# Kernel tuning notes

Hardware: AMD Instinct MI355X
Metric: run time of the kernel (lower is better)

The kernel has to match this reference:

```python
import jax, jax.numpy as jnp
import numpy as np

N_NODES = 50000
EPS = 1e-16
NEG_SLOPE = 0.2


def _gat_conv(x, src, dst, W, a_src, a_dst, bias, heads, out_c, concat, n):
    # Linear transform: [N, heads, out_c]
    h = (x @ W).reshape(n, heads, out_c)
    # Per-node attention logits (split form of PyG's 'a' vector)
    al_src = jnp.einsum('nhc,hc->nh', h, a_src)  # [N, H]
    al_dst = jnp.einsum('nhc,hc->nh', h, a_dst)  # [N, H]
    # Edge-wise scores, softmax over incoming edges of each destination
    e = jax.nn.leaky_relu(al_src[src] + al_dst[dst], NEG_SLOPE)  # [E, H]
    m = jax.ops.segment_max(e, dst, num_segments=n)              # [N, H]
    ex = jnp.exp(e - m[dst])
    s = jax.ops.segment_sum(ex, dst, num_segments=n)             # [N, H]
    alpha = ex / (s[dst] + EPS)                                  # [E, H]
    # Attention-weighted scatter-aggregate of source features
    out = jax.ops.segment_sum(h[src] * alpha[:, :, None], dst, num_segments=n)
    if concat:
        out = out.reshape(n, heads * out_c)
    else:
        out = out.mean(axis=1)
    return out + bias


def _add_self_loops(edge_index, n):
    loop = jnp.arange(n, dtype=edge_index.dtype)
    src = jnp.concatenate([edge_index[0], loop])
    dst = jnp.concatenate([edge_index[1], loop])
    return src, dst


def setup_inputs() -> dict:
    key = jax.random.key(0)
    ks = jax.random.split(key, 10)
    n, e = N_NODES, 640000
    x = jax.random.normal(ks[0], (n, 128), dtype=jnp.float32)
    edge_index = jax.random.randint(ks[1], (2, e), 0, n, dtype=jnp.int64)
    sc = 0.1
    return {
        'x': x,
        'edge_index': edge_index,
        'W1': jax.random.normal(ks[2], (128, 256), dtype=jnp.float32) * sc,
        'a1_src': jax.random.normal(ks[3], (8, 32), dtype=jnp.float32) * sc,
        'a1_dst': jax.random.normal(ks[4], (8, 32), dtype=jnp.float32) * sc,
        'b1': jax.random.normal(ks[5], (256,), dtype=jnp.float32) * sc,
        'W2': jax.random.normal(ks[6], (256, 64), dtype=jnp.float32) * sc,
        'a2_src': jax.random.normal(ks[7], (1, 64), dtype=jnp.float32) * sc,
        'a2_dst': jax.random.normal(ks[8], (1, 64), dtype=jnp.float32) * sc,
        'b2': jax.random.normal(ks[9], (64,), dtype=jnp.float32) * sc,
    }


def reference(x, edge_index, W1, a1_src, a1_dst, b1, W2, a2_src, a2_dst, b2):
    n = x.shape[0]
    src, dst = _add_self_loops(edge_index, n)  # PyG GATConv add_self_loops=True
    # Dropouts are identity in eval mode.
    h = _gat_conv(x, src, dst, W1, a1_src, a1_dst, b1, heads=8, out_c=32, concat=True, n=n)
    h = jax.nn.elu(h)
    out = _gat_conv(h, src, dst, W2, a2_src, a2_dst, b2, heads=1, out_c=64, concat=False, n=n)
    return out
```

## Files before the change

### kernel.cpp

```cpp
#include <hip/hip_runtime.h>


static __device__ __forceinline__ float lrelu(float x) { return x > 0.f ? x : 0.2f * x; }

__global__ void count_deg(const int* __restrict__ dstv, int* __restrict__ deg, int E) {
  int e = blockIdx.x * blockDim.x + threadIdx.x;
  if (e < E) atomicAdd(&deg[dstv[e]], 1);
}

__global__ void scan_partial(const int* __restrict__ deg, int* __restrict__ off,
                             int* __restrict__ bsum, int n) {
  int tid = threadIdx.x;
  int i = blockIdx.x * 256 + tid;
  int v = (i < n) ? deg[i] : 0;
  int lane = tid & 63, w = tid >> 6;
  int sv = v;
#pragma unroll
  for (int o = 1; o < 64; o <<= 1) {
    int t = __shfl_up(sv, o);
    if (lane >= o) sv += t;
  }
  __shared__ int ws[4];
  if (lane == 63) ws[w] = sv;
  __syncthreads();
  int add = 0;
  for (int j = 0; j < w; ++j) add += ws[j];
  sv += add;
  if (i < n) off[i + 1] = sv;
  if (tid == 255) bsum[blockIdx.x] = sv;
}

__global__ void scan_bsum(int* __restrict__ bsum, int* __restrict__ off, int nb) {
  int tid = threadIdx.x;
  int v = (tid < nb) ? bsum[tid] : 0;
  int lane = tid & 63, w = tid >> 6;
  int sv = v;
#pragma unroll
  for (int o = 1; o < 64; o <<= 1) {
    int t = __shfl_up(sv, o);
    if (lane >= o) sv += t;
  }
  __shared__ int ws[4];
  if (lane == 63) ws[w] = sv;
  __syncthreads();
  int add = 0;
  for (int j = 0; j < w; ++j) add += ws[j];
  sv += add;
  if (tid < nb) bsum[tid] = sv - v;
  if (tid == 0) off[0] = 0;
}

__global__ void add_carry(const int* __restrict__ deg, int* __restrict__ off,
                          const int* __restrict__ bsum, int* __restrict__ cur, int n) {
  int i = blockIdx.x * 256 + threadIdx.x;
  if (i < n) {
    int o = off[i + 1] + bsum[blockIdx.x];
    off[i + 1] = o;
    cur[i] = o - deg[i];
  }
}

__global__ void fill_csr(const int* __restrict__ srcv, const int* __restrict__ dstv,
                         int* __restrict__ cur, int* __restrict__ csr,
                         int* __restrict__ csr_dst, int E) {
  int e = blockIdx.x * blockDim.x + threadIdx.x;
  if (e < E) {
    int d = dstv[e];
    int p = atomicAdd(&cur[d], 1);
    csr[p] = srcv[e];
    csr_dst[p] = d;
  }
}

__global__ __launch_bounds__(256) void gemm1(const float* __restrict__ x, const float* __restrict__ W,
                                             float* __restrict__ h, int n) {
  __shared__ float xs[32][64];
  __shared__ float Ws[32][256];
  int tid = threadIdx.x;
  int tc = tid & 31;
  int tr = tid >> 5;
  int lr = tid & 63, lj = tid >> 6;
  int r0 = blockIdx.x * 64;

  float acc[8][8];
#pragma unroll
  for (int r = 0; r < 8; ++r)
#pragma unroll
    for (int j = 0; j < 8; ++j) acc[r][j] = 0.f;

  for (int k0 = 0; k0 < 128; k0 += 32) {
    __syncthreads();
    {
      int rr = r0 + lr;
      float4 v0 = {0, 0, 0, 0}, v1 = {0, 0, 0, 0};
      if (rr < n) {
        const float* p = x + (size_t)rr * 128 + k0 + lj * 8;
        v0 = *(const float4*)p;
        v1 = *(const float4*)(p + 4);
      }
      int kk = lj * 8;
      xs[kk + 0][lr] = v0.x; xs[kk + 1][lr] = v0.y; xs[kk + 2][lr] = v0.z; xs[kk + 3][lr] = v0.w;
      xs[kk + 4][lr] = v1.x; xs[kk + 5][lr] = v1.y; xs[kk + 6][lr] = v1.z; xs[kk + 7][lr] = v1.w;
    }
    {
      const float4* src = (const float4*)(W + (size_t)k0 * 256);
      float4* dst = (float4*)&Ws[0][0];
#pragma unroll
      for (int i = tid; i < 2048; i += 256) dst[i] = src[i];
    }
    __syncthreads();
#pragma unroll 4
    for (int k = 0; k < 32; ++k) {
      float xv[8];
      *(float4*)&xv[0] = *(const float4*)&xs[k][tr * 8];
      *(float4*)&xv[4] = *(const float4*)&xs[k][tr * 8 + 4];
      float wv[8];
#pragma unroll
      for (int j = 0; j < 8; ++j) wv[j] = Ws[k][tc + 32 * j];
#pragma unroll
      for (int r = 0; r < 8; ++r)
#pragma unroll
        for (int j = 0; j < 8; ++j) acc[r][j] = fmaf(xv[r], wv[j], acc[r][j]);
    }
  }
#pragma unroll
  for (int r = 0; r < 8; ++r) {
    int row = r0 + tr * 8 + r;
    if (row < n) {
#pragma unroll
      for (int j = 0; j < 8; ++j) h[(size_t)row * 256 + tc + 32 * j] = acc[r][j];
    }
  }
}

__global__ __launch_bounds__(256) void gemm2(const float* __restrict__ xin, const float* __restrict__ W,
                                             float* __restrict__ h, int n) {
  __shared__ float xs[32][128];
  __shared__ float Ws[32][64];
  int tid = threadIdx.x;
  int tc = tid & 15;
  int tr = tid >> 4;
  int r0 = blockIdx.x * 128;

  float acc[8][4];
#pragma unroll
  for (int r = 0; r < 8; ++r)
#pragma unroll
    for (int j = 0; j < 4; ++j) acc[r][j] = 0.f;

  for (int k0 = 0; k0 < 256; k0 += 32) {
    __syncthreads();
#pragma unroll
    for (int idx = tid; idx < 1024; idx += 256) {
      int r = idx & 127, q = idx >> 7;
      int rr = r0 + r;
      float4 v = {0, 0, 0, 0};
      if (rr < n) v = *(const float4*)(xin + (size_t)rr * 256 + k0 + q * 4);
      int kk = q * 4;
      xs[kk + 0][r] = v.x; xs[kk + 1][r] = v.y; xs[kk + 2][r] = v.z; xs[kk + 3][r] = v.w;
    }
    {
      const float4* src = (const float4*)(W + (size_t)k0 * 64);
      float4* dst = (float4*)&Ws[0][0];
#pragma unroll
      for (int i = tid; i < 512; i += 256) dst[i] = src[i];
    }
    __syncthreads();
#pragma unroll 4
    for (int k = 0; k < 32; ++k) {
      float xv[8];
      *(float4*)&xv[0] = *(const float4*)&xs[k][tr * 8];
      *(float4*)&xv[4] = *(const float4*)&xs[k][tr * 8 + 4];
      float wv[4];
#pragma unroll
      for (int j = 0; j < 4; ++j) wv[j] = Ws[k][tc + 16 * j];
#pragma unroll
      for (int r = 0; r < 8; ++r)
#pragma unroll
        for (int j = 0; j < 4; ++j) acc[r][j] = fmaf(xv[r], wv[j], acc[r][j]);
    }
  }
#pragma unroll
  for (int r = 0; r < 8; ++r) {
    int row = r0 + tr * 8 + r;
    if (row < n) {
#pragma unroll
      for (int j = 0; j < 4; ++j) h[(size_t)row * 64 + tc + 16 * j] = acc[r][j];
    }
  }
}

__global__ __launch_bounds__(256) void logits1(const float* __restrict__ h, const float* __restrict__ as,
                                               const float* __restrict__ ad, float* __restrict__ als,
                                               float* __restrict__ ald, int n) {
  int node = blockIdx.x * 4 + (threadIdx.x >> 6);
  int lane = threadIdx.x & 63;
  if (node >= n) return;
  float4 v = *(const float4*)&h[(size_t)node * 256 + lane * 4];
  float4 cs = *(const float4*)&as[lane * 4];
  float4 cd = *(const float4*)&ad[lane * 4];
  float ps = v.x * cs.x + v.y * cs.y + v.z * cs.z + v.w * cs.w;
  float pd = v.x * cd.x + v.y * cd.y + v.z * cd.z + v.w * cd.w;
#pragma unroll
  for (int o = 1; o < 8; o <<= 1) {
    ps += __shfl_xor(ps, o);
    pd += __shfl_xor(pd, o);
  }
  if ((lane & 7) == 0) {
    int head = lane >> 3;
    als[node * 8 + head] = ps;
    ald[node * 8 + head] = pd;
  }
}

__global__ __launch_bounds__(256) void logits2(const float* __restrict__ h, const float* __restrict__ as,
                                               const float* __restrict__ ad, float* __restrict__ als,
                                               float* __restrict__ ald, int n) {
  int node = blockIdx.x * 4 + (threadIdx.x >> 6);
  int lane = threadIdx.x & 63;
  if (node >= n) return;
  float v = h[(size_t)node * 64 + lane];
  float ps = v * as[lane];
  float pd = v * ad[lane];
#pragma unroll
  for (int o = 1; o < 64; o <<= 1) {
    ps += __shfl_xor(ps, o);
    pd += __shfl_xor(pd, o);
  }
  if (lane == 0) {
    als[node] = ps;
    ald[node] = pd;
  }
}

__global__ __launch_bounds__(256) void alpha1_k(const float* __restrict__ als, const float* __restrict__ ald,
                                                const int* __restrict__ csr, const int* __restrict__ csr_dst,
                                                float* __restrict__ alpha, int E) {
  int idx = blockIdx.x * 256 + threadIdx.x;
  if (idx >= E * 8) return;
  int p = idx >> 3, hd = idx & 7;
  int s = csr[p], d = csr_dst[p];
  alpha[idx] = expf(lrelu(als[s * 8 + hd] + ald[d * 8 + hd]));
}

__global__ __launch_bounds__(256) void alpha2_k(const float* __restrict__ als, const float* __restrict__ ald,
                                                const int* __restrict__ csr, const int* __restrict__ csr_dst,
                                                float* __restrict__ alpha, int E) {
  int p = blockIdx.x * 256 + threadIdx.x;
  if (p >= E) return;
  alpha[p] = expf(lrelu(als[csr[p]] + ald[csr_dst[p]]));
}

__global__ __launch_bounds__(256) void agg1(const float* __restrict__ h, const float* __restrict__ alpha,
                                            const float* __restrict__ als, const float* __restrict__ ald,
                                            const int* __restrict__ off, const int* __restrict__ csr,
                                            const float* __restrict__ bias, float* __restrict__ outp, int n) {
  int d = blockIdx.x * 4 + (threadIdx.x >> 6);
  if (d >= n) return;
  int lane = threadIdx.x & 63;
  int head = lane >> 3;
  float w0 = expf(lrelu(als[d * 8 + head] + ald[d * 8 + head]));
  float4 hv = *(const float4*)&h[(size_t)d * 256 + lane * 4];
  float4 acc;
  acc.x = w0 * hv.x; acc.y = w0 * hv.y; acc.z = w0 * hv.z; acc.w = w0 * hv.w;
  float wsum = w0;
  int beg = off[d], end = off[d + 1];
  int i = beg;
  for (; i + 1 < end; i += 2) {
    int s0 = csr[i], s1 = csr[i + 1];
    float wa = alpha[(size_t)i * 8 + head];
    float wb = alpha[(size_t)(i + 1) * 8 + head];
    float4 h0 = *(const float4*)&h[(size_t)s0 * 256 + lane * 4];
    float4 h1 = *(const float4*)&h[(size_t)s1 * 256 + lane * 4];
    acc.x = fmaf(wa, h0.x, acc.x); acc.y = fmaf(wa, h0.y, acc.y);
    acc.z = fmaf(wa, h0.z, acc.z); acc.w = fmaf(wa, h0.w, acc.w);
    acc.x = fmaf(wb, h1.x, acc.x); acc.y = fmaf(wb, h1.y, acc.y);
    acc.z = fmaf(wb, h1.z, acc.z); acc.w = fmaf(wb, h1.w, acc.w);
    wsum += wa + wb;
  }
  if (i < end) {
    int s = csr[i];
    float w = alpha[(size_t)i * 8 + head];
    float4 h0 = *(const float4*)&h[(size_t)s * 256 + lane * 4];
    acc.x = fmaf(w, h0.x, acc.x); acc.y = fmaf(w, h0.y, acc.y);
    acc.z = fmaf(w, h0.z, acc.z); acc.w = fmaf(w, h0.w, acc.w);
    wsum += w;
  }
  float inv = 1.f / (wsum + 1e-16f);
  float4 b = *(const float4*)&bias[lane * 4];
  float4 o;
  o.x = acc.x * inv + b.x; o.y = acc.y * inv + b.y;
  o.z = acc.z * inv + b.z; o.w = acc.w * inv + b.w;
  o.x = o.x > 0.f ? o.x : expm1f(o.x);
  o.y = o.y > 0.f ? o.y : expm1f(o.y);
  o.z = o.z > 0.f ? o.z : expm1f(o.z);
  o.w = o.w > 0.f ? o.w : expm1f(o.w);
  *(float4*)&outp[(size_t)d * 256 + lane * 4] = o;
}

__global__ __launch_bounds__(256) void agg2(const float* __restrict__ h, const float* __restrict__ alpha,
                                            const float* __restrict__ als, const float* __restrict__ ald,
                                            const int* __restrict__ off, const int* __restrict__ csr,
                                            const float* __restrict__ bias, float* __restrict__ outp, int n) {
  int d = blockIdx.x * 4 + (threadIdx.x >> 6);
  if (d >= n) return;
  int c = threadIdx.x & 63;
  float w0 = expf(lrelu(als[d] + ald[d]));
  float acc = w0 * h[(size_t)d * 64 + c];
  float wsum = w0;
  int beg = off[d], end = off[d + 1];
  int i = beg;
  for (; i + 1 < end; i += 2) {
    int s0 = csr[i], s1 = csr[i + 1];
    float wa = alpha[i];
    float wb = alpha[i + 1];
    float h0 = h[(size_t)s0 * 64 + c];
    float h1 = h[(size_t)s1 * 64 + c];
    acc = fmaf(wa, h0, acc);
    acc = fmaf(wb, h1, acc);
    wsum += wa + wb;
  }
  if (i < end) {
    int s = csr[i];
    float w = alpha[i];
    acc = fmaf(w, h[(size_t)s * 64 + c], acc);
    wsum += w;
  }
  outp[(size_t)d * 64 + c] = acc / (wsum + 1e-16f) + bias[c];
}

extern "C" void kernel_launch(void* const* d_in, const int* in_sizes, int n_in,
                              void* d_out, int out_size, void* d_ws, size_t ws_size,
                              hipStream_t stream) {
  const float* x  = (const float*)d_in[0];
  const int* ei   = (const int*)d_in[1];
  const float* W1 = (const float*)d_in[2];
  const float* a1s = (const float*)d_in[3];
  const float* a1d = (const float*)d_in[4];
  const float* b1  = (const float*)d_in[5];
  const float* W2  = (const float*)d_in[6];
  const float* a2s = (const float*)d_in[7];
  const float* a2d = (const float*)d_in[8];
  const float* b2  = (const float*)d_in[9];
  float* outp = (float*)d_out;

  int n = in_sizes[0] / 128;
  int E = in_sizes[1] / 2;
  const int* srcv = ei;
  const int* dstv = ei + E;

  char* wsb = (char*)d_ws;
  size_t p = 0;
  auto alloc = [&](size_t bytes) -> char* {
    char* r = wsb + p;
    p += (bytes + 511) & ~size_t(511);
    return r;
  };
  int* deg  = (int*)alloc((size_t)n * 4);
  int* off  = (int*)alloc(((size_t)n + 1) * 4);
  int* cur  = (int*)alloc((size_t)n * 4);
  int* bsum = (int*)alloc(1024);
  int* csr  = (int*)alloc((size_t)E * 4);
  int* csrd = (int*)alloc((size_t)E * 4);
  float* h1   = (float*)alloc((size_t)n * 256 * 4);
  float* al1s = (float*)alloc((size_t)n * 8 * 4);
  float* al1d = (float*)alloc((size_t)n * 8 * 4);
  float* o1   = (float*)alloc((size_t)n * 256 * 4);
  float* h2   = (float*)alloc((size_t)n * 64 * 4);
  float* al2s = (float*)alloc((size_t)n * 4);
  float* al2d = (float*)alloc((size_t)n * 4);
  float* alp1 = (float*)alloc((size_t)E * 8 * 4);
  float* alp2 = (float*)alloc((size_t)E * 4);
  (void)ws_size;

  hipMemsetAsync(deg, 0, (size_t)n * 4, stream);
  int eb = (E + 255) / 256;
  int nb = (n + 255) / 256;
  count_deg<<<eb, 256, 0, stream>>>(dstv, deg, E);
  scan_partial<<<nb, 256, 0, stream>>>(deg, off, bsum, n);
  scan_bsum<<<1, 256, 0, stream>>>(bsum, off, nb);
  add_carry<<<nb, 256, 0, stream>>>(deg, off, bsum, cur, n);
  fill_csr<<<eb, 256, 0, stream>>>(srcv, dstv, cur, csr, csrd, E);

  gemm1<<<(n + 63) / 64, 256, 0, stream>>>(x, W1, h1, n);
  logits1<<<(n + 3) / 4, 256, 0, stream>>>(h1, a1s, a1d, al1s, al1d, n);
  alpha1_k<<<(E * 8 + 255) / 256, 256, 0, stream>>>(al1s, al1d, csr, csrd, alp1, E);
  agg1<<<(n + 3) / 4, 256, 0, stream>>>(h1, alp1, al1s, al1d, off, csr, b1, o1, n);
  gemm2<<<(n + 127) / 128, 256, 0, stream>>>(o1, W2, h2, n);
  logits2<<<(n + 3) / 4, 256, 0, stream>>>(h2, a2s, a2d, al2s, al2d, n);
  alpha2_k<<<eb, 256, 0, stream>>>(al2s, al2d, csr, csrd, alp2, E);
  agg2<<<(n + 3) / 4, 256, 0, stream>>>(h2, alp2, al2s, al2d, off, csr, b2, outp, n);
}
```

Measured before the change: 436.8 us.

## Fuse edge attention weight computation into aggregation kernels, drop alpha buffers

Removes the separate alpha1/alpha2 kernels and the per-edge alpha and csr_dst arrays, and computes exp(leaky_relu(als[src]+ald[dst])) inline inside the aggregation loops. This avoids writing and re-reading E*8 and E floats plus the destination-index array, and drops two launches. In exchange each lane recomputes the exp redundantly and does an extra gather of als per source. The aggregation loops are also unrolled from 2 to 4 edges to expose more memory-level parallelism.

```diff
diff --git a/kernel.cpp b/kernel.cpp
--- a/kernel.cpp
+++ b/kernel.cpp
@@ -61,14 +61,11 @@
 }
 
 __global__ void fill_csr(const int* __restrict__ srcv, const int* __restrict__ dstv,
-                         int* __restrict__ cur, int* __restrict__ csr,
-                         int* __restrict__ csr_dst, int E) {
+                         int* __restrict__ cur, int* __restrict__ csr, int E) {
   int e = blockIdx.x * blockDim.x + threadIdx.x;
   if (e < E) {
-    int d = dstv[e];
-    int p = atomicAdd(&cur[d], 1);
+    int p = atomicAdd(&cur[dstv[e]], 1);
     csr[p] = srcv[e];
-    csr_dst[p] = d;
   }
 }
 
@@ -233,25 +230,7 @@
   }
 }
 
-__global__ __launch_bounds__(256) void alpha1_k(const float* __restrict__ als, const float* __restrict__ ald,
-                                                const int* __restrict__ csr, const int* __restrict__ csr_dst,
-                                                float* __restrict__ alpha, int E) {
-  int idx = blockIdx.x * 256 + threadIdx.x;
-  if (idx >= E * 8) return;
-  int p = idx >> 3, hd = idx & 7;
-  int s = csr[p], d = csr_dst[p];
-  alpha[idx] = expf(lrelu(als[s * 8 + hd] + ald[d * 8 + hd]));
-}
-
-__global__ __launch_bounds__(256) void alpha2_k(const float* __restrict__ als, const float* __restrict__ ald,
-                                                const int* __restrict__ csr, const int* __restrict__ csr_dst,
-                                                float* __restrict__ alpha, int E) {
-  int p = blockIdx.x * 256 + threadIdx.x;
-  if (p >= E) return;
-  alpha[p] = expf(lrelu(als[csr[p]] + ald[csr_dst[p]]));
-}
-
-__global__ __launch_bounds__(256) void agg1(const float* __restrict__ h, const float* __restrict__ alpha,
+__global__ __launch_bounds__(256) void agg1(const float* __restrict__ h,
                                             const float* __restrict__ als, const float* __restrict__ ald,
                                             const int* __restrict__ off, const int* __restrict__ csr,
                                             const float* __restrict__ bias, float* __restrict__ outp, int n) {
@@ -259,28 +238,41 @@
   if (d >= n) return;
   int lane = threadIdx.x & 63;
   int head = lane >> 3;
-  float w0 = expf(lrelu(als[d * 8 + head] + ald[d * 8 + head]));
+  float ad = ald[d * 8 + head];
+  float w0 = expf(lrelu(als[d * 8 + head] + ad));
   float4 hv = *(const float4*)&h[(size_t)d * 256 + lane * 4];
   float4 acc;
   acc.x = w0 * hv.x; acc.y = w0 * hv.y; acc.z = w0 * hv.z; acc.w = w0 * hv.w;
   float wsum = w0;
   int beg = off[d], end = off[d + 1];
   int i = beg;
-  for (; i + 1 < end; i += 2) {
-    int s0 = csr[i], s1 = csr[i + 1];
-    float wa = alpha[(size_t)i * 8 + head];
-    float wb = alpha[(size_t)(i + 1) * 8 + head];
+  for (; i + 3 < end; i += 4) {
+    int s0 = csr[i], s1 = csr[i + 1], s2 = csr[i + 2], s3 = csr[i + 3];
+    float a0 = als[s0 * 8 + head];
+    float a1 = als[s1 * 8 + head];
+    float a2 = als[s2 * 8 + head];
+    float a3 = als[s3 * 8 + head];
     float4 h0 = *(const float4*)&h[(size_t)s0 * 256 + lane * 4];
     float4 h1 = *(const float4*)&h[(size_t)s1 * 256 + lane * 4];
+    float4 h2 = *(const float4*)&h[(size_t)s2 * 256 + lane * 4];
+    float4 h3 = *(const float4*)&h[(size_t)s3 * 256 + lane * 4];
+    float wa = expf(lrelu(a0 + ad));
+    float wb = expf(lrelu(a1 + ad));
+    float wc = expf(lrelu(a2 + ad));
+    float wd = expf(lrelu(a3 + ad));
     acc.x = fmaf(wa, h0.x, acc.x); acc.y = fmaf(wa, h0.y, acc.y);
     acc.z = fmaf(wa, h0.z, acc.z); acc.w = fmaf(wa, h0.w, acc.w);
     acc.x = fmaf(wb, h1.x, acc.x); acc.y = fmaf(wb, h1.y, acc.y);
     acc.z = fmaf(wb, h1.z, acc.z); acc.w = fmaf(wb, h1.w, acc.w);
-    wsum += wa + wb;
-  }
-  if (i < end) {
+    acc.x = fmaf(wc, h2.x, acc.x); acc.y = fmaf(wc, h2.y, acc.y);
+    acc.z = fmaf(wc, h2.z, acc.z); acc.w = fmaf(wc, h2.w, acc.w);
+    acc.x = fmaf(wd, h3.x, acc.x); acc.y = fmaf(wd, h3.y, acc.y);
+    acc.z = fmaf(wd, h3.z, acc.z); acc.w = fmaf(wd, h3.w, acc.w);
+    wsum += (wa + wb) + (wc + wd);
+  }
+  for (; i < end; ++i) {
     int s = csr[i];
-    float w = alpha[(size_t)i * 8 + head];
+    float w = expf(lrelu(als[s * 8 + head] + ad));
     float4 h0 = *(const float4*)&h[(size_t)s * 256 + lane * 4];
     acc.x = fmaf(w, h0.x, acc.x); acc.y = fmaf(w, h0.y, acc.y);
     acc.z = fmaf(w, h0.z, acc.z); acc.w = fmaf(w, h0.w, acc.w);
@@ -298,31 +290,42 @@
   *(float4*)&outp[(size_t)d * 256 + lane * 4] = o;
 }
 
-__global__ __launch_bounds__(256) void agg2(const float* __restrict__ h, const float* __restrict__ alpha,
+__global__ __launch_bounds__(256) void agg2(const float* __restrict__ h,
                                             const float* __restrict__ als, const float* __restrict__ ald,
                                             const int* __restrict__ off, const int* __restrict__ csr,
                                             const float* __restrict__ bias, float* __restrict__ outp, int n) {
   int d = blockIdx.x * 4 + (threadIdx.x >> 6);
   if (d >= n) return;
   int c = threadIdx.x & 63;
-  float w0 = expf(lrelu(als[d] + ald[d]));
+  float ad = ald[d];
+  float w0 = expf(lrelu(als[d] + ad));
   float acc = w0 * h[(size_t)d * 64 + c];
   float wsum = w0;
   int beg = off[d], end = off[d + 1];
   int i = beg;
-  for (; i + 1 < end; i += 2) {
-    int s0 = csr[i], s1 = csr[i + 1];
-    float wa = alpha[i];
-    float wb = alpha[i + 1];
+  for (; i + 3 < end; i += 4) {
+    int s0 = csr[i], s1 = csr[i + 1], s2 = csr[i + 2], s3 = csr[i + 3];
+    float a0 = als[s0];
+    float a1 = als[s1];
+    float a2 = als[s2];
+    float a3 = als[s3];
     float h0 = h[(size_t)s0 * 64 + c];
     float h1 = h[(size_t)s1 * 64 + c];
+    float h2 = h[(size_t)s2 * 64 + c];
+    float h3 = h[(size_t)s3 * 64 + c];
+    float wa = expf(lrelu(a0 + ad));
+    float wb = expf(lrelu(a1 + ad));
+    float wc = expf(lrelu(a2 + ad));
+    float wd = expf(lrelu(a3 + ad));
     acc = fmaf(wa, h0, acc);
     acc = fmaf(wb, h1, acc);
-    wsum += wa + wb;
-  }
-  if (i < end) {
+    acc = fmaf(wc, h2, acc);
+    acc = fmaf(wd, h3, acc);
+    wsum += (wa + wb) + (wc + wd);
+  }
+  for (; i < end; ++i) {
     int s = csr[i];
-    float w = alpha[i];
+    float w = expf(lrelu(als[s] + ad));
     acc = fmaf(w, h[(size_t)s * 64 + c], acc);
     wsum += w;
   }
@@ -361,7 +364,6 @@
   int* cur  = (int*)alloc((size_t)n * 4);
   int* bsum = (int*)alloc(1024);
   int* csr  = (int*)alloc((size_t)E * 4);
-  int* csrd = (int*)alloc((size_t)E * 4);
   float* h1   = (float*)alloc((size_t)n * 256 * 4);
   float* al1s = (float*)alloc((size_t)n * 8 * 4);
   float* al1d = (float*)alloc((size_t)n * 8 * 4);
@@ -369,8 +371,6 @@
   float* h2   = (float*)alloc((size_t)n * 64 * 4);
   float* al2s = (float*)alloc((size_t)n * 4);
   float* al2d = (float*)alloc((size_t)n * 4);
-  float* alp1 = (float*)alloc((size_t)E * 8 * 4);
-  float* alp2 = (float*)alloc((size_t)E * 4);
   (void)ws_size;
 
   hipMemsetAsync(deg, 0, (size_t)n * 4, stream);
@@ -380,14 +380,12 @@
   scan_partial<<<nb, 256, 0, stream>>>(deg, off, bsum, n);
   scan_bsum<<<1, 256, 0, stream>>>(bsum, off, nb);
   add_carry<<<nb, 256, 0, stream>>>(deg, off, bsum, cur, n);
-  fill_csr<<<eb, 256, 0, stream>>>(srcv, dstv, cur, csr, csrd, E);
+  fill_csr<<<eb, 256, 0, stream>>>(srcv, dstv, cur, csr, E);
 
   gemm1<<<(n + 63) / 64, 256, 0, stream>>>(x, W1, h1, n);
   logits1<<<(n + 3) / 4, 256, 0, stream>>>(h1, a1s, a1d, al1s, al1d, n);
-  alpha1_k<<<(E * 8 + 255) / 256, 256, 0, stream>>>(al1s, al1d, csr, csrd, alp1, E);
-  agg1<<<(n + 3) / 4, 256, 0, stream>>>(h1, alp1, al1s, al1d, off, csr, b1, o1, n);
+  agg1<<<(n + 3) / 4, 256, 0, stream>>>(h1, al1s, al1d, off, csr, b1, o1, n);
   gemm2<<<(n + 127) / 128, 256, 0, stream>>>(o1, W2, h2, n);
   logits2<<<(n + 3) / 4, 256, 0, stream>>>(h2, a2s, a2d, al2s, al2d, n);
-  alpha2_k<<<eb, 256, 0, stream>>>(al2s, al2d, csr, csrd, alp2, E);
-  agg2<<<(n + 3) / 4, 256, 0, stream>>>(h2, alp2, al2s, al2d, off, csr, b2, outp, n);
-}
+  agg2<<<(n + 3) / 4, 256, 0, stream>>>(h2, al2s, al2d, off, csr, b2, outp, n);
+}
```

Result: faster. 410.5 us (-6.0%).
